# Kernel tuning notes

Measured on AMD Instinct MI355X. Metric: run time of the kernel, lower is better.

## Reference

```python
import jax, jax.numpy as jnp
import numpy as np

B, N, INPUT, HIDDEN, WEIGHT = 1024, 50, 128, 256, 64
NEG_INF = -1.0e9


def setup_inputs() -> dict:
    key = jax.random.key(0)
    ks = jax.random.split(key, 12)
    s_in = 1.0 / np.sqrt(INPUT)
    s_h = 1.0 / np.sqrt(HIDDEN)
    s_w = 1.0 / np.sqrt(WEIGHT)
    return {
        "targets": jax.random.normal(ks[0], (B, N, INPUT), jnp.float32),
        "h0": jax.random.normal(ks[1], (B, HIDDEN), jnp.float32),
        "c0": jax.random.normal(ks[2], (B, HIDDEN), jnp.float32),
        # nn.Linear(input_size, hidden_size)
        "W_enc": jax.random.uniform(ks[3], (HIDDEN, INPUT), jnp.float32, -s_in, s_in),
        "b_enc": jax.random.uniform(ks[4], (HIDDEN,), jnp.float32, -s_in, s_in),
        # nn.LSTMCell(input_size, hidden_size)
        "W_ih": jax.random.uniform(ks[5], (4 * HIDDEN, INPUT), jnp.float32, -s_h, s_h),
        "W_hh": jax.random.uniform(ks[6], (4 * HIDDEN, HIDDEN), jnp.float32, -s_h, s_h),
        "b_ih": jax.random.uniform(ks[7], (4 * HIDDEN,), jnp.float32, -s_h, s_h),
        "b_hh": jax.random.uniform(ks[8], (4 * HIDDEN,), jnp.float32, -s_h, s_h),
        # W1, W2: Linear(hidden, weight, bias=False); vt: Linear(weight, 1, bias=False)
        "W1": jax.random.uniform(ks[9], (WEIGHT, HIDDEN), jnp.float32, -s_h, s_h),
        "W2": jax.random.uniform(ks[10], (WEIGHT, HIDDEN), jnp.float32, -s_h, s_h),
        "vt": jax.random.uniform(ks[11], (WEIGHT,), jnp.float32, -s_w, s_w),
    }


def _lstm_cell(x, h, c, W_ih, W_hh, b_ih, b_hh):
    gates = x @ W_ih.T + h @ W_hh.T + (b_ih + b_hh)  # [B, 4H]
    i, f, g, o = jnp.split(gates, 4, axis=-1)
    i, f, o = jax.nn.sigmoid(i), jax.nn.sigmoid(f), jax.nn.sigmoid(o)
    g = jnp.tanh(g)
    c_new = f * c + i * g
    h_new = o * jnp.tanh(c_new)
    return h_new, c_new


def _pointer_forward(targets, h0, c0, W_enc, b_enc, W_ih, W_hh, b_ih, b_hh, W1, W2, vt):
    b, n, _ = targets.shape
    encoder_states = targets @ W_enc.T + b_enc        # [B, N, H]
    blend1 = encoder_states @ W1.T                    # [B, N, W]
    col = jnp.arange(n)

    def step(carry, _):
        h, c, dec_in, selected = carry
        h, c = _lstm_cell(dec_in, h, c, W_ih, W_hh, b_ih, b_hh)
        blend2 = h @ W2.T                             # [B, W]
        out = jnp.tanh(blend1 + blend2[:, None, :]) @ vt  # [B, N]
        out = jnp.where(selected, NEG_INF, out)
        sel_idx = jnp.argmax(out, axis=-1)            # [B]
        selected = selected | (col[None, :] == sel_idx[:, None])
        p = jnp.maximum(jax.nn.softmax(out, axis=-1), 1e-9)
        dec_in = targets[jnp.arange(b), sel_idx]      # gather next input
        return (h, c, dec_in, selected), p

    dec_in0 = jnp.zeros_like(targets[:, 0])
    selected0 = jnp.zeros((b, n), dtype=bool)
    _, probs = jax.lax.scan(step, (h0, c0, dec_in0, selected0), None, length=n)
    return jnp.transpose(probs, (1, 0, 2))            # [B, N, N]


def reference(targets, h0, c0, W_enc, b_enc, W_ih, W_hh, b_ih, b_hh, W1, W2, vt):
    return _pointer_forward(targets, h0, c0, W_enc, b_enc, W_ih, W_hh, b_ih, b_hh, W1, W2, vt)
```

## Files before the change

kernel.cpp:

```cpp
#include <hip/hip_runtime.h>

#define O_WC     16
#define O_BC     (16 + 8192)
#define O_BIAS   (O_BC + 64)
#define O_BLEND1 16384
#define O_WB     3293184
#define O_XW     4194304
#define XW_FLOATS 52428800ULL
#define NEG_INF_V (-1.0e9f)

#define WB_TILE 12288
#define WB_W2   786432

using bf16x8 = __attribute__((ext_vector_type(8))) __bf16;
using f32x4  = __attribute__((ext_vector_type(4))) float;

__device__ __forceinline__ f32x4 mfma16(bf16x8 a, bf16x8 b, f32x4 c) {
  return __builtin_amdgcn_mfma_f32_16x16x32_bf16(a, b, c, 0, 0, 0);
}

__device__ __forceinline__ float b2f(unsigned int u) {
  union { unsigned int i; float f; } x; x.i = u << 16; return x.f;
}
__device__ __forceinline__ unsigned short f2b(float f) {
  union { float f; unsigned int i; } x; x.f = f;
  unsigned int r = x.i + 0x7fffu + ((x.i >> 16) & 1u);
  return (unsigned short)(r >> 16);
}
__device__ __forceinline__ float ldv(const void* p, int b16, long long i) {
  if (b16) return b2f(((const unsigned short*)p)[i]);
  return ((const float*)p)[i];
}
__device__ __forceinline__ float sigm(float x)  { return 1.0f / (1.0f + __expf(-x)); }
__device__ __forceinline__ float tanhx(float x) { return 1.0f - 2.0f / (1.0f + __expf(2.0f * x)); }

__device__ __forceinline__ float bfsel(const uint4& u, int e) {
  unsigned int w = (e < 2) ? u.x : (e < 4) ? u.y : (e < 6) ? u.z : u.w;
  union { unsigned int i; float f; } x;
  x.i = (e & 1) ? (w & 0xffff0000u) : (w << 16);
  return x.f;
}

__global__ __launch_bounds__(256) void prepAll(
    const void* b_enc, const void* b_ih, const void* b_hh, const void* W1,
    const void* W_ih, const void* W_hh, const void* W2, float* ws) {
  __shared__ int anybig;
  const int t = threadIdx.x;
  const int blk = blockIdx.x;
  if (t == 0) anybig = 0;
  __syncthreads();
  {
    unsigned short u = ((const unsigned short*)b_enc)[t];
    float f = b2f((unsigned int)u);
    if (!(fabsf(f) <= 1.0f)) atomicOr(&anybig, 1);
  }
  __syncthreads();
  const int b16 = anybig ? 0 : 1;

  if (blk == 0) {
    if (t == 0) ((int*)ws)[0] = b16;
    for (int k = t; k < 1024; k += 256)
      ws[O_BIAS + k] = ldv(b_ih, b16, k) + ldv(b_hh, b16, k);
    if (t < 64) {
      float acc = 0.f;
      for (int h = 0; h < 256; ++h)
        acc += ldv(W1, b16, t * 256 + h) * ldv(b_enc, b16, h);
      ws[O_BC + t] = acc;
    }
  }
  if (blk < 32) {
  }
  unsigned short* wb = (unsigned short*)(ws + O_WB);
  const int i = blk * 256 + t;
  {
    int g = i >> 8, k = i & 255;
    int nt = g >> 4, r = g & 15;
    int kc = k >> 5, lane = ((k >> 3) & 3) * 16 + r, e = k & 7;
    float w = ldv(W_hh, b16, i);
    unsigned short hi = f2b(w);
    long long d = (long long)nt * WB_TILE + kc * 512 + lane * 8 + e;
    wb[d] = hi;
    wb[d + 4096] = f2b(w - b2f((unsigned int)hi));
  }
  if (i < 131072) {
    int g = i >> 7, k = i & 127;
    int nt = g >> 4, r = g & 15;
    int kc = k >> 5, lane = ((k >> 3) & 3) * 16 + r, e = k & 7;
    float w = ldv(W_ih, b16, i);
    unsigned short hi = f2b(w);
    long long d = (long long)nt * WB_TILE + 8192 + kc * 512 + lane * 8 + e;
    wb[d] = hi;
    wb[d + 2048] = f2b(w - b2f((unsigned int)hi));
  }
  if (i < 16384) {
    int g = i >> 8, k = i & 255;
    int ntw = g >> 4, r = g & 15;
    int kc = k >> 5, lane = ((k >> 3) & 3) * 16 + r, e = k & 7;
    float w = ldv(W2, b16, i);
    unsigned short hi = f2b(w);
    long long d = WB_W2 + ntw * 8192 + kc * 512 + lane * 8 + e;
    wb[d] = hi;
    wb[d + 4096] = f2b(w - b2f((unsigned int)hi));
  }
}

__global__ void prep1(const void* W_enc, const void* W1, const void* b_enc,
                      float* ws) {
  __shared__ int anybig;
  int t = threadIdx.x;
  if (t == 0) anybig = 0;
  __syncthreads();
  {
    unsigned short u = ((const unsigned short*)b_enc)[t];
    float f = b2f((unsigned int)u);
    if (!(fabsf(f) <= 1.0f)) atomicOr(&anybig, 1);
  }
  __syncthreads();
  int b16 = anybig ? 0 : 1;
  int o = blockIdx.x * 256 + t;
  int w = o >> 7, i = o & 127;
  float acc = 0.f;
  for (int h = 0; h < 256; ++h)
    acc += ldv(W1, b16, w * 256 + h) * ldv(W_enc, b16, h * 128 + i);
  ws[O_WC + o] = acc;
}

__global__ __launch_bounds__(256) void blendk(const void* targets, float* ws) {
  __shared__ float tg[6400];
  __shared__ float wc[8192];
  int b16 = ((const int*)ws)[0];
  int t = threadIdx.x, b = blockIdx.x;
  for (int k = t; k < 8192; k += 256) wc[k] = ws[O_WC + k];
  if (b16) {
    const unsigned short* tp = (const unsigned short*)targets + (long long)b * 6400;
    for (int k = t * 8; k < 6400; k += 2048) {
      uint4 u = *(const uint4*)(tp + k);
      #pragma unroll
      for (int e = 0; e < 8; ++e) tg[k + e] = bfsel(u, e);
    }
  } else {
    const float* tp = (const float*)targets + (long long)b * 6400;
    for (int k = t; k < 6400; k += 256) tg[k] = tp[k];
  }
  __syncthreads();
  int w = t & 63, j0 = t >> 6;
  float bcv = ws[O_BC + w];
  for (int j = j0; j < 50; j += 4) {
    float acc = 0.f;
    for (int i0 = 0; i0 < 128; i0 += 8) {
      const float4* q = (const float4*)(wc + w * 128 + i0);
      float4 a = q[0], bb = q[1];
      const float* x = &tg[j * 128 + i0];
      acc += a.x * x[0] + a.y * x[1] + a.z * x[2] + a.w * x[3]
           + bb.x * x[4] + bb.y * x[5] + bb.z * x[6] + bb.w * x[7];
    }
    ws[O_BLEND1 + (b * 50 + j) * 64 + w] = acc + bcv;
  }
}

__global__ __launch_bounds__(512)
__attribute__((amdgpu_waves_per_eu(2, 2)))
void xwK(const void* targets, float* ws) {
  __shared__ __align__(16) unsigned short tgS[4][32][264];
  const int b16 = ((const int*)ws)[0];
  const int t = threadIdx.x;
  const int b0 = blockIdx.x * 4;
  const unsigned short* wb = (const unsigned short*)(ws + O_WB);
  float* xwp = ws + O_XW;
  const int l = t & 63, Wv = t >> 6, lr = l & 15, hc = l >> 4;

  #pragma unroll 1
  for (int half = 0; half < 2; ++half) {
    __syncthreads();
    for (int k = t; k < 4 * 32 * 128; k += 512) {
      int p = k >> 12, jr = (k >> 7) & 31, i = k & 127;
      int j = half * 32 + jr;
      float v = (j < 50) ? ldv(targets, b16, ((long long)(b0 + p) * 50 + j) * 128 + i)
                         : 0.f;
      unsigned short hi = f2b(v);
      tgS[p][jr][i]       = hi;
      tgS[p][jr][128 + i] = f2b(v - b2f((unsigned int)hi));
    }
    __syncthreads();
    const int njg = (half == 0) ? 4 : 3;
    #pragma unroll 1
    for (int ti = 0; ti < 8; ++ti) {
      const int nt = Wv * 8 + ti;
      const unsigned short* tb = wb + (long long)nt * WB_TILE + 8192 + l * 8;
      bf16x8 wih[8];
      #pragma unroll
      for (int kc = 0; kc < 4; ++kc) {
        wih[kc]     = *(const bf16x8*)(tb + kc * 512);
        wih[4 + kc] = *(const bf16x8*)(tb + 2048 + kc * 512);
      }
      #pragma unroll 1
      for (int p = 0; p < 4; ++p) {
        #pragma unroll 1
        for (int jh = 0; jh < njg; ++jh) {
          bf16x8 ax[4];
          const unsigned short* tp =
              &tgS[p][jh * 8 + (lr & 7)][((lr < 8) ? 0 : 128) + hc * 8];
          #pragma unroll
          for (int kc = 0; kc < 4; ++kc) ax[kc] = *(const bf16x8*)(tp + kc * 32);
          f32x4 cH = {0.f,0.f,0.f,0.f}, cL = {0.f,0.f,0.f,0.f};
          #pragma unroll
          for (int kc = 0; kc < 4; ++kc) {
            cH = mfma16(ax[kc], wih[kc], cH);
            cL = mfma16(ax[kc], wih[4 + kc], cL);
          }
          f32x4 acc = cH + cL;
          float s0 = acc[0] + __shfl_xor(acc[0], 32, 64);
          float s1 = acc[1] + __shfl_xor(acc[1], 32, 64);
          float s2 = acc[2] + __shfl_xor(acc[2], 32, 64);
          float s3 = acc[3] + __shfl_xor(acc[3], 32, 64);
          if (l < 32) {
            int jb = half * 32 + jh * 8 + hc * 4;
            long long ro = (long long)(b0 + p) * 50;
            if (jb + 0 < 50) xwp[(ro + jb + 0) * 1024 + nt * 16 + lr] = s0;
            if (jb + 1 < 50) xwp[(ro + jb + 1) * 1024 + nt * 16 + lr] = s1;
            if (jb + 2 < 50) xwp[(ro + jb + 2) * 1024 + nt * 16 + lr] = s2;
            if (jb + 3 < 50) xwp[(ro + jb + 3) * 1024 + nt * 16 + lr] = s3;
          }
        }
      }
    }
  }
}

__global__ __launch_bounds__(1024)
__attribute__((amdgpu_waves_per_eu(4, 4)))
void mainX(const void* targets, const void* h0, const void* c0, const void* vt,
           float* ws, void* outp) {
  __shared__ __align__(16) unsigned short hS[16][264];
  __shared__ __align__(16) float xwS[4][1024];
  __shared__ float cT[4][256];
  __shared__ float gsh[4][1024];
  __shared__ float bias_s[1024];
  __shared__ float b2s[4][64];
  __shared__ float outs[4][64];
  __shared__ float vt_s[64];
  __shared__ int   selidx[4];
  __shared__ int   selb[4][64];

  const int b16 = ((const int*)ws)[0];
  const int t = threadIdx.x;
  const int bbase = blockIdx.x * 4;
  const unsigned short* wb = (const unsigned short*)(ws + O_WB);
  const float* xw = ws + O_XW;

  bias_s[t & 1023] = ws[O_BIAS + (t & 1023)];
  if (t < 64) vt_s[t] = ldv(vt, b16, t);
  if (t < 256) selb[t >> 6][t & 63] = 0;
  if (t < 4) selidx[t] = -1;
  {
    unsigned short* z1 = &hS[0][0];
    for (int k = t; k < 16 * 264; k += 1024) z1[k] = 0;
  }
  __syncthreads();
  {
    int p = t >> 8, j = t & 255;
    float h = ldv(h0, b16, (long long)(bbase + p) * 256 + j);
    float c = ldv(c0, b16, (long long)(bbase + p) * 256 + j);
    unsigned short hi = f2b(h);
    hS[p][j]     = hi;
    hS[p + 4][j] = f2b(h - b2f((unsigned int)hi));
    cT[p][j]     = c;
  }
  __syncthreads();

  const int l  = t & 63, Wv = t >> 6;
  const int lr = l & 15, hc = l >> 4;

  float bl1[16];
  int cp = 0, cj = 0, cq = 0;
  if (t < 800) {
    int o = t >> 2; cq = t & 3;
    cp = o / 50; cj = o - cp * 50;
    const float* bl = ws + O_BLEND1 + (((long long)(bbase + cp) * 50 + cj) * 64) + cq * 16;
    #pragma unroll
    for (int v4 = 0; v4 < 4; ++v4) {
      float4 bv = *(const float4*)(bl + v4 * 4);
      bl1[v4 * 4 + 0] = bv.x; bl1[v4 * 4 + 1] = bv.y;
      bl1[v4 * 4 + 2] = bv.z; bl1[v4 * 4 + 3] = bv.w;
    }
  } else {
    #pragma unroll
    for (int e = 0; e < 16; ++e) bl1[e] = 0.f;
  }

  #pragma unroll 1
  for (int step = 0; step < 50; ++step) {
    {
      bf16x8 ah[8];
      #pragma unroll
      for (int kc = 0; kc < 8; ++kc)
        ah[kc] = *(const bf16x8*)&hS[lr][kc * 32 + hc * 8];
      #pragma unroll 1
      for (int ti = 0; ti < 4; ++ti) {
        const int nt = Wv * 4 + ti;
        const unsigned short* tb = wb + (long long)nt * WB_TILE + l * 8;
        bf16x8 wh[4], wl[4];
        #pragma unroll
        for (int q2 = 0; q2 < 4; ++q2) {
          wh[q2] = *(const bf16x8*)(tb + q2 * 512);
          wl[q2] = *(const bf16x8*)(tb + 4096 + q2 * 512);
        }
        f32x4 aH = {0.f,0.f,0.f,0.f}, aL = {0.f,0.f,0.f,0.f};
        #pragma unroll
        for (int kc = 0; kc < 8; ++kc) {
          const int cur = kc & 3;
          aH = mfma16(ah[kc], wh[cur], aH);
          aL = mfma16(ah[kc], wl[cur], aL);
          if (kc + 4 < 8) {
            wh[cur] = *(const bf16x8*)(tb + (kc + 4) * 512);
            wl[cur] = *(const bf16x8*)(tb + 4096 + (kc + 4) * 512);
          }
        }
        f32x4 acc = aH + aL;
        float s0 = acc[0] + __shfl_xor(acc[0], 16, 64);
        float s1 = acc[1] + __shfl_xor(acc[1], 16, 64);
        float s2 = acc[2] + __shfl_xor(acc[2], 16, 64);
        float s3 = acc[3] + __shfl_xor(acc[3], 16, 64);
        if (l < 16) {
          const int g = nt * 16 + l;
          gsh[0][g] = s0; gsh[1][g] = s1; gsh[2][g] = s2; gsh[3][g] = s3;
        }
      }
    }
    __syncthreads();

    {
      int j = t & 255, p = t >> 8;
      float gi = gsh[p][j], gf = gsh[p][256 + j];
      float gg = gsh[p][512 + j], go = gsh[p][768 + j];
      if (selidx[p] >= 0) {
        gi += xwS[p][j]; gf += xwS[p][256 + j];
        gg += xwS[p][512 + j]; go += xwS[p][768 + j];
      }
      gi = sigm (gi + bias_s[j]);
      gf = sigm (gf + bias_s[256 + j]);
      gg = tanhx(gg + bias_s[512 + j]);
      go = sigm (go + bias_s[768 + j]);
      float c = gf * cT[p][j] + gi * gg;
      cT[p][j] = c;
      float h = go * tanhx(c);
      unsigned short hi = f2b(h);
      hS[p][j]     = hi;
      hS[p + 4][j] = f2b(h - b2f((unsigned int)hi));
    }
    __syncthreads();

    if (Wv < 4) {
      bf16x8 bh[8];
      #pragma unroll
      for (int kc = 0; kc < 8; ++kc)
        bh[kc] = *(const bf16x8*)&hS[lr][kc * 32 + hc * 8];
      const unsigned short* tb2 = wb + WB_W2 + Wv * 8192 + l * 8;
      f32x4 cH = {0.f,0.f,0.f,0.f}, cL = {0.f,0.f,0.f,0.f};
      #pragma unroll
      for (int kc = 0; kc < 8; ++kc) {
        cH = mfma16(bh[kc], *(const bf16x8*)(tb2 + kc * 512), cH);
        cL = mfma16(bh[kc], *(const bf16x8*)(tb2 + 4096 + kc * 512), cL);
      }
      f32x4 acc = cH + cL;
      float s0 = acc[0] + __shfl_xor(acc[0], 16, 64);
      float s1 = acc[1] + __shfl_xor(acc[1], 16, 64);
      float s2 = acc[2] + __shfl_xor(acc[2], 16, 64);
      float s3 = acc[3] + __shfl_xor(acc[3], 16, 64);
      if (l < 16) {
        const int g = Wv * 16 + l;
        b2s[0][g] = s0; b2s[1][g] = s1; b2s[2][g] = s2; b2s[3][g] = s3;
      }
    }
    __syncthreads();

    if (t < 800) {
      float acc = 0.f;
      #pragma unroll
      for (int e = 0; e < 16; ++e) {
        int w0 = cq * 16 + e;
        acc += vt_s[w0] * tanhx(bl1[e] + b2s[cp][w0]);
      }
      acc += __shfl_xor(acc, 1, 64);
      acc += __shfl_xor(acc, 2, 64);
      if (cq == 0) outs[cp][cj] = selb[cp][cj] ? NEG_INF_V : acc;
    }
    __syncthreads();

    if (Wv < 4) {
      int p = Wv, lane = l;
      float v = (lane < 50) ? outs[p][lane] : -3.4e38f;
      int idx = lane;
      #pragma unroll
      for (int msk = 1; msk < 64; msk <<= 1) {
        float ov = __shfl_xor(v, msk, 64);
        int   oi = __shfl_xor(idx, msk, 64);
        if (ov > v || (ov == v && oi < idx)) { v = ov; idx = oi; }
      }
      {
        const float* xr = xw + ((long long)(bbase + p) * 50 + idx) * 1024;
        #pragma unroll
        for (int kk = 0; kk < 4; ++kk)
          *(float4*)&xwS[p][lane * 4 + kk * 256] =
              *(const float4*)(xr + lane * 4 + kk * 256);
      }
      float e = (lane < 50) ? __expf(outs[p][lane] - v) : 0.f;
      float ssum = e;
      #pragma unroll
      for (int msk = 1; msk < 64; msk <<= 1) ssum += __shfl_xor(ssum, msk, 64);
      if (lane < 50) {
        float prob = fmaxf(e / ssum, 1e-9f);
        long long o = (long long)(bbase + p) * 2500 + step * 50 + lane;
        if (b16) ((unsigned short*)outp)[o] = f2b(prob);
        else     ((float*)outp)[o] = prob;
      }
      if (lane == 0) selidx[p] = idx;
      if (lane == idx) selb[p][idx] = 1;
    }
    __syncthreads();
  }
}

__global__ __launch_bounds__(512)
__attribute__((amdgpu_waves_per_eu(2, 2)))
void mainK6(const void* targets, const void* h0, const void* c0, const void* vt,
            float* ws, void* outp) {
  __shared__ __align__(16) unsigned short hS[16][264];
  __shared__ __align__(16) unsigned short xA[16][136];
  __shared__ float cT[8][256];
  __shared__ float gsh[8][1024];
  __shared__ float bias_s[1024];
  __shared__ float b2s[8][64];
  __shared__ float outs[8][64];
  __shared__ float vt_s[64];
  __shared__ int   selidx[8];
  __shared__ int   selb[8][64];

  const int b16 = ((const int*)ws)[0];
  const int t = threadIdx.x;
  const int bbase = blockIdx.x * 8;
  const unsigned short* wb = (const unsigned short*)(ws + O_WB);

  for (int k = t; k < 1024; k += 512) bias_s[k] = ws[O_BIAS + k];
  if (t < 64) vt_s[t] = ldv(vt, b16, t);
  if (t < 512) selb[t >> 6][t & 63] = 0;
  if (t < 8) selidx[t] = -1;
  {
    unsigned short* z1 = &hS[0][0];
    unsigned short* z2 = &xA[0][0];
    for (int k = t; k < 16 * 264; k += 512) z1[k] = 0;
    for (int k = t; k < 16 * 136; k += 512) z2[k] = 0;
  }
  __syncthreads();
  for (int k = t; k < 2048; k += 512) {
    int p = k >> 8, j = k & 255;
    float h = ldv(h0, b16, (long long)(bbase + p) * 256 + j);
    float c = ldv(c0, b16, (long long)(bbase + p) * 256 + j);
    unsigned short hi = f2b(h);
    hS[p][j]     = hi;
    hS[p + 8][j] = f2b(h - b2f((unsigned int)hi));
    cT[p][j]     = c;
  }
  __syncthreads();

  const int l  = t & 63, Wv = t >> 6;
  const int lr = l & 15;

  #pragma unroll 1
  for (int step = 0; step < 50; ++step) {
    {
      bf16x8 ah[8], ax[4];
      #pragma unroll
      for (int kc = 0; kc < 8; ++kc)
        ah[kc] = *(const bf16x8*)&hS[lr][kc * 32 + (l >> 4) * 8];
      #pragma unroll
      for (int kc = 0; kc < 4; ++kc)
        ax[kc] = *(const bf16x8*)&xA[lr][kc * 32 + (l >> 4) * 8];
      #pragma unroll 1
      for (int ti = 0; ti < 8; ++ti) {
        const int nt = Wv * 8 + ti;
        const unsigned short* tb = wb + (long long)nt * WB_TILE + l * 8;
        bf16x8 wH[12], wL[12];
        #pragma unroll
        for (int kc = 0; kc < 8; ++kc) {
          wH[kc] = *(const bf16x8*)(tb + kc * 512);
          wL[kc] = *(const bf16x8*)(tb + 4096 + kc * 512);
        }
        #pragma unroll
        for (int kc = 0; kc < 4; ++kc) {
          wH[8 + kc] = *(const bf16x8*)(tb + 8192 + kc * 512);
          wL[8 + kc] = *(const bf16x8*)(tb + 10240 + kc * 512);
        }
        f32x4 aH = {0.f,0.f,0.f,0.f}, aL = {0.f,0.f,0.f,0.f};
        #pragma unroll
        for (int kc = 0; kc < 8; ++kc) {
          aH = mfma16(ah[kc], wH[kc], aH);
          aL = mfma16(ah[kc], wL[kc], aL);
        }
        #pragma unroll
        for (int kc = 0; kc < 4; ++kc) {
          aH = mfma16(ax[kc], wH[8 + kc], aH);
          aL = mfma16(ax[kc], wL[8 + kc], aL);
        }
        f32x4 acc = aH + aL;
        float s0 = acc[0] + __shfl_xor(acc[0], 32, 64);
        float s1 = acc[1] + __shfl_xor(acc[1], 32, 64);
        float s2 = acc[2] + __shfl_xor(acc[2], 32, 64);
        float s3 = acc[3] + __shfl_xor(acc[3], 32, 64);
        if (l < 32) {
          const int g = nt * 16 + (l & 15), pb = (l >> 4) * 4;
          gsh[pb + 0][g] = s0; gsh[pb + 1][g] = s1;
          gsh[pb + 2][g] = s2; gsh[pb + 3][g] = s3;
        }
      }
    }
    __syncthreads();

    for (int k = t; k < 2048; k += 512) {
      int j = k & 255, p = k >> 8;
      float gi = sigm (gsh[p][j]       + bias_s[j]);
      float gf = sigm (gsh[p][256 + j] + bias_s[256 + j]);
      float gg = tanhx(gsh[p][512 + j] + bias_s[512 + j]);
      float go = sigm (gsh[p][768 + j] + bias_s[768 + j]);
      float c = gf * cT[p][j] + gi * gg;
      cT[p][j] = c;
      float h = go * tanhx(c);
      unsigned short hi = f2b(h);
      hS[p][j]     = hi;
      hS[p + 8][j] = f2b(h - b2f((unsigned int)hi));
    }
    __syncthreads();

    if (Wv < 4) {
      bf16x8 bh[8];
      #pragma unroll
      for (int kc = 0; kc < 8; ++kc)
        bh[kc] = *(const bf16x8*)&hS[lr][kc * 32 + (l >> 4) * 8];
      const unsigned short* tb = wb + WB_W2 + Wv * 8192 + l * 8;
      f32x4 aH = {0.f,0.f,0.f,0.f}, aL = {0.f,0.f,0.f,0.f};
      #pragma unroll
      for (int kc = 0; kc < 8; ++kc) {
        aH = mfma16(bh[kc], *(const bf16x8*)(tb + kc * 512), aH);
        aL = mfma16(bh[kc], *(const bf16x8*)(tb + 4096 + kc * 512), aL);
      }
      f32x4 acc = aH + aL;
      float s0 = acc[0] + __shfl_xor(acc[0], 32, 64);
      float s1 = acc[1] + __shfl_xor(acc[1], 32, 64);
      float s2 = acc[2] + __shfl_xor(acc[2], 32, 64);
      float s3 = acc[3] + __shfl_xor(acc[3], 32, 64);
      if (l < 32) {
        const int g = Wv * 16 + (l & 15), pb = (l >> 4) * 4;
        b2s[pb + 0][g] = s0; b2s[pb + 1][g] = s1;
        b2s[pb + 2][g] = s2; b2s[pb + 3][g] = s3;
      }
    }
    __syncthreads();

    if (t < 400) {
      int p = t / 50, j = t - p * 50;
      const float* bl = ws + O_BLEND1 + (((bbase + p) * 50 + j) * 64);
      float acc = 0.f;
      #pragma unroll
      for (int v4 = 0; v4 < 16; ++v4) {
        float4 bv = *(const float4*)(bl + v4 * 4);
        int w0 = v4 * 4;
        acc += vt_s[w0 + 0] * tanhx(bv.x + b2s[p][w0 + 0]);
        acc += vt_s[w0 + 1] * tanhx(bv.y + b2s[p][w0 + 1]);
        acc += vt_s[w0 + 2] * tanhx(bv.z + b2s[p][w0 + 2]);
        acc += vt_s[w0 + 3] * tanhx(bv.w + b2s[p][w0 + 3]);
      }
      outs[p][j] = selb[p][j] ? NEG_INF_V : acc;
    }
    __syncthreads();

    {
      int p = Wv, lane = l;
      float v = (lane < 50) ? outs[p][lane] : -3.4e38f;
      int idx = lane;
      #pragma unroll
      for (int msk = 1; msk < 64; msk <<= 1) {
        float ov = __shfl_xor(v, msk, 64);
        int   oi = __shfl_xor(idx, msk, 64);
        if (ov > v || (ov == v && oi < idx)) { v = ov; idx = oi; }
      }
      float e = (lane < 50) ? __expf(outs[p][lane] - v) : 0.f;
      float ssum = e;
      #pragma unroll
      for (int msk = 1; msk < 64; msk <<= 1) ssum += __shfl_xor(ssum, msk, 64);
      if (lane < 50) {
        float prob = fmaxf(e / ssum, 1e-9f);
        int o = (bbase + p) * 2500 + step * 50 + lane;
        if (b16) ((unsigned short*)outp)[o] = f2b(prob);
        else     ((float*)outp)[o] = prob;
      }
      if (lane == 0) selidx[p] = idx;
      if (lane == idx) selb[p][idx] = 1;
    }
    __syncthreads();

    for (int k = t; k < 1024; k += 512) {
      int p = k >> 7, i = k & 127;
      float xf = ldv(targets, b16,
                     ((long long)(bbase + p) * 50 + selidx[p]) * 128 + i);
      unsigned short hi = f2b(xf);
      xA[p][i]     = hi;
      xA[p + 8][i] = f2b(xf - b2f((unsigned int)hi));
    }
    __syncthreads();
  }
}

extern "C" void kernel_launch(void* const* d_in, const int* in_sizes, int n_in,
                              void* d_out, int out_size, void* d_ws, size_t ws_size,
                              hipStream_t stream) {
  (void)in_sizes; (void)n_in; (void)out_size;
  const void* targets = d_in[0];
  const void* h0      = d_in[1];
  const void* c0      = d_in[2];
  const void* W_enc   = d_in[3];
  const void* b_enc   = d_in[4];
  const void* W_ih    = d_in[5];
  const void* W_hh    = d_in[6];
  const void* b_ih    = d_in[7];
  const void* b_hh    = d_in[8];
  const void* W1      = d_in[9];
  const void* W2      = d_in[10];
  const void* vt      = d_in[11];
  float* ws = (float*)d_ws;

  int use_xw = (ws_size >= ((size_t)O_XW + (size_t)XW_FLOATS) * 4) ? 1 : 0;

  prepAll<<<1024, 256, 0, stream>>>(b_enc, b_ih, b_hh, W1, W_ih, W_hh, W2, ws);
  prep1<<<32, 256, 0, stream>>>(W_enc, W1, b_enc, ws);
  blendk<<<1024, 256, 0, stream>>>(targets, ws);
  if (use_xw) {
    xwK<<<256, 512, 0, stream>>>(targets, ws);
    mainX<<<256, 1024, 0, stream>>>(targets, h0, c0, vt, ws, d_out);
  } else {
    mainK6<<<128, 512, 0, stream>>>(targets, h0, c0, vt, ws, d_out);
  }
}
```

Measured before the change: 991.8 us.

## Overlap next-step recurrent GEMM with attention/softmax via warp specialization

Splits the 16 waves of mainX into two groups. 12 waves compute the next step's h·W_hh gate GEMM while 4 waves compute blend2, the attention scores, argmax, softmax and the gather. The small group synchronises internally through a shared-memory atomic counter with spin-sleep, which removes several block-wide barriers per step. Blend1 is staged in shared memory instead of per-thread registers, and the first step's GEMM is hoisted before the loop. The costs are more shared memory use, a spin-wait, and more score work per lane (64 tanh per lane instead of 16).

```diff
diff --git a/kernel.cpp b/kernel.cpp
--- a/kernel.cpp
+++ b/kernel.cpp
@@ -67,8 +67,6 @@
         acc += ldv(W1, b16, t * 256 + h) * ldv(b_enc, b16, h);
       ws[O_BC + t] = acc;
     }
-  }
-  if (blk < 32) {
   }
   unsigned short* wb = (unsigned short*)(ws + O_WB);
   const int i = blk * 256 + t;
@@ -233,14 +231,15 @@
            float* ws, void* outp) {
   __shared__ __align__(16) unsigned short hS[16][264];
   __shared__ __align__(16) float xwS[4][1024];
+  __shared__ float bl1S[4][50][66];
   __shared__ float cT[4][256];
   __shared__ float gsh[4][1024];
   __shared__ float bias_s[1024];
   __shared__ float b2s[4][64];
-  __shared__ float outs[4][64];
   __shared__ float vt_s[64];
   __shared__ int   selidx[4];
   __shared__ int   selb[4][64];
+  __shared__ int   auxcnt;
 
   const int b16 = ((const int*)ws)[0];
   const int t = threadIdx.x;
@@ -248,13 +247,18 @@
   const unsigned short* wb = (const unsigned short*)(ws + O_WB);
   const float* xw = ws + O_XW;
 
-  bias_s[t & 1023] = ws[O_BIAS + (t & 1023)];
+  bias_s[t] = ws[O_BIAS + t];
   if (t < 64) vt_s[t] = ldv(vt, b16, t);
   if (t < 256) selb[t >> 6][t & 63] = 0;
   if (t < 4) selidx[t] = -1;
+  if (t == 0) auxcnt = 0;
   {
     unsigned short* z1 = &hS[0][0];
     for (int k = t; k < 16 * 264; k += 1024) z1[k] = 0;
+  }
+  for (int k = t; k < 12800; k += 1024) {
+    int p = k / 3200, r = k - p * 3200, j = r >> 6, w = r & 63;
+    bl1S[p][j][w] = ws[O_BLEND1 + (((long long)(bbase + p) * 50 + j) << 6) + w];
   }
   __syncthreads();
   {
@@ -271,64 +275,46 @@
   const int l  = t & 63, Wv = t >> 6;
   const int lr = l & 15, hc = l >> 4;
 
-  float bl1[16];
-  int cp = 0, cj = 0, cq = 0;
-  if (t < 800) {
-    int o = t >> 2; cq = t & 3;
-    cp = o / 50; cj = o - cp * 50;
-    const float* bl = ws + O_BLEND1 + (((long long)(bbase + cp) * 50 + cj) * 64) + cq * 16;
+  {
+    bf16x8 ah[8];
     #pragma unroll
-    for (int v4 = 0; v4 < 4; ++v4) {
-      float4 bv = *(const float4*)(bl + v4 * 4);
-      bl1[v4 * 4 + 0] = bv.x; bl1[v4 * 4 + 1] = bv.y;
-      bl1[v4 * 4 + 2] = bv.z; bl1[v4 * 4 + 3] = bv.w;
-    }
-  } else {
-    #pragma unroll
-    for (int e = 0; e < 16; ++e) bl1[e] = 0.f;
-  }
+    for (int kc = 0; kc < 8; ++kc)
+      ah[kc] = *(const bf16x8*)&hS[lr][kc * 32 + hc * 8];
+    #pragma unroll 1
+    for (int nt = Wv; nt < 64; nt += 16) {
+      const unsigned short* tb = wb + (long long)nt * WB_TILE + l * 8;
+      bf16x8 wh[4], wl[4];
+      #pragma unroll
+      for (int q2 = 0; q2 < 4; ++q2) {
+        wh[q2] = *(const bf16x8*)(tb + q2 * 512);
+        wl[q2] = *(const bf16x8*)(tb + 4096 + q2 * 512);
+      }
+      f32x4 aH = {0.f,0.f,0.f,0.f}, aL = {0.f,0.f,0.f,0.f};
+      #pragma unroll
+      for (int kc = 0; kc < 8; ++kc) {
+        const int cur = kc & 3;
+        aH = mfma16(ah[kc], wh[cur], aH);
+        aL = mfma16(ah[kc], wl[cur], aL);
+        if (kc + 4 < 8) {
+          wh[cur] = *(const bf16x8*)(tb + (kc + 4) * 512);
+          wl[cur] = *(const bf16x8*)(tb + 4096 + (kc + 4) * 512);
+        }
+      }
+      f32x4 acc = aH + aL;
+      float s0 = acc[0] + __shfl_xor(acc[0], 16, 64);
+      float s1 = acc[1] + __shfl_xor(acc[1], 16, 64);
+      float s2 = acc[2] + __shfl_xor(acc[2], 16, 64);
+      float s3 = acc[3] + __shfl_xor(acc[3], 16, 64);
+      if (l < 16) {
+        const int g = nt * 16 + l;
+        gsh[0][g] = s0; gsh[1][g] = s1; gsh[2][g] = s2; gsh[3][g] = s3;
+      }
+    }
+  }
+  __syncthreads();
 
   #pragma unroll 1
   for (int step = 0; step < 50; ++step) {
-    {
-      bf16x8 ah[8];
-      #pragma unroll
-      for (int kc = 0; kc < 8; ++kc)
-        ah[kc] = *(const bf16x8*)&hS[lr][kc * 32 + hc * 8];
-      #pragma unroll 1
-      for (int ti = 0; ti < 4; ++ti) {
-        const int nt = Wv * 4 + ti;
-        const unsigned short* tb = wb + (long long)nt * WB_TILE + l * 8;
-        bf16x8 wh[4], wl[4];
-        #pragma unroll
-        for (int q2 = 0; q2 < 4; ++q2) {
-          wh[q2] = *(const bf16x8*)(tb + q2 * 512);
-          wl[q2] = *(const bf16x8*)(tb + 4096 + q2 * 512);
-        }
-        f32x4 aH = {0.f,0.f,0.f,0.f}, aL = {0.f,0.f,0.f,0.f};
-        #pragma unroll
-        for (int kc = 0; kc < 8; ++kc) {
-          const int cur = kc & 3;
-          aH = mfma16(ah[kc], wh[cur], aH);
-          aL = mfma16(ah[kc], wl[cur], aL);
-          if (kc + 4 < 8) {
-            wh[cur] = *(const bf16x8*)(tb + (kc + 4) * 512);
-            wl[cur] = *(const bf16x8*)(tb + 4096 + (kc + 4) * 512);
-          }
-        }
-        f32x4 acc = aH + aL;
-        float s0 = acc[0] + __shfl_xor(acc[0], 16, 64);
-        float s1 = acc[1] + __shfl_xor(acc[1], 16, 64);
-        float s2 = acc[2] + __shfl_xor(acc[2], 16, 64);
-        float s3 = acc[3] + __shfl_xor(acc[3], 16, 64);
-        if (l < 16) {
-          const int g = nt * 16 + l;
-          gsh[0][g] = s0; gsh[1][g] = s1; gsh[2][g] = s2; gsh[3][g] = s3;
-        }
-      }
-    }
-    __syncthreads();
-
     {
       int j = t & 255, p = t >> 8;
       float gi = gsh[p][j], gf = gsh[p][256 + j];
@@ -350,72 +336,112 @@
     }
     __syncthreads();
 
-    if (Wv < 4) {
-      bf16x8 bh[8];
-      #pragma unroll
-      for (int kc = 0; kc < 8; ++kc)
-        bh[kc] = *(const bf16x8*)&hS[lr][kc * 32 + hc * 8];
-      const unsigned short* tb2 = wb + WB_W2 + Wv * 8192 + l * 8;
-      f32x4 cH = {0.f,0.f,0.f,0.f}, cL = {0.f,0.f,0.f,0.f};
-      #pragma unroll
-      for (int kc = 0; kc < 8; ++kc) {
-        cH = mfma16(bh[kc], *(const bf16x8*)(tb2 + kc * 512), cH);
-        cL = mfma16(bh[kc], *(const bf16x8*)(tb2 + 4096 + kc * 512), cL);
-      }
-      f32x4 acc = cH + cL;
-      float s0 = acc[0] + __shfl_xor(acc[0], 16, 64);
-      float s1 = acc[1] + __shfl_xor(acc[1], 16, 64);
-      float s2 = acc[2] + __shfl_xor(acc[2], 16, 64);
-      float s3 = acc[3] + __shfl_xor(acc[3], 16, 64);
-      if (l < 16) {
-        const int g = Wv * 16 + l;
-        b2s[0][g] = s0; b2s[1][g] = s1; b2s[2][g] = s2; b2s[3][g] = s3;
-      }
-    }
-    __syncthreads();
-
-    if (t < 800) {
-      float acc = 0.f;
-      #pragma unroll
-      for (int e = 0; e < 16; ++e) {
-        int w0 = cq * 16 + e;
-        acc += vt_s[w0] * tanhx(bl1[e] + b2s[cp][w0]);
-      }
-      acc += __shfl_xor(acc, 1, 64);
-      acc += __shfl_xor(acc, 2, 64);
-      if (cq == 0) outs[cp][cj] = selb[cp][cj] ? NEG_INF_V : acc;
-    }
-    __syncthreads();
-
-    if (Wv < 4) {
-      int p = Wv, lane = l;
-      float v = (lane < 50) ? outs[p][lane] : -3.4e38f;
-      int idx = lane;
-      #pragma unroll
-      for (int msk = 1; msk < 64; msk <<= 1) {
-        float ov = __shfl_xor(v, msk, 64);
-        int   oi = __shfl_xor(idx, msk, 64);
-        if (ov > v || (ov == v && oi < idx)) { v = ov; idx = oi; }
-      }
+    if (Wv >= 4) {
+      if (step < 49) {
+        bf16x8 ah[8];
+        #pragma unroll
+        for (int kc = 0; kc < 8; ++kc)
+          ah[kc] = *(const bf16x8*)&hS[lr][kc * 32 + hc * 8];
+        #pragma unroll 1
+        for (int nt = Wv - 4; nt < 64; nt += 12) {
+          const unsigned short* tb = wb + (long long)nt * WB_TILE + l * 8;
+          bf16x8 wh[4], wl[4];
+          #pragma unroll
+          for (int q2 = 0; q2 < 4; ++q2) {
+            wh[q2] = *(const bf16x8*)(tb + q2 * 512);
+            wl[q2] = *(const bf16x8*)(tb + 4096 + q2 * 512);
+          }
+          f32x4 aH = {0.f,0.f,0.f,0.f}, aL = {0.f,0.f,0.f,0.f};
+          #pragma unroll
+          for (int kc = 0; kc < 8; ++kc) {
+            const int cur = kc & 3;
+            aH = mfma16(ah[kc], wh[cur], aH);
+            aL = mfma16(ah[kc], wl[cur], aL);
+            if (kc + 4 < 8) {
+              wh[cur] = *(const bf16x8*)(tb + (kc + 4) * 512);
+              wl[cur] = *(const bf16x8*)(tb + 4096 + (kc + 4) * 512);
+            }
+          }
+          f32x4 acc = aH + aL;
+          float s0 = acc[0] + __shfl_xor(acc[0], 16, 64);
+          float s1 = acc[1] + __shfl_xor(acc[1], 16, 64);
+          float s2 = acc[2] + __shfl_xor(acc[2], 16, 64);
+          float s3 = acc[3] + __shfl_xor(acc[3], 16, 64);
+          if (l < 16) {
+            const int g = nt * 16 + l;
+            gsh[0][g] = s0; gsh[1][g] = s1; gsh[2][g] = s2; gsh[3][g] = s3;
+          }
+        }
+      }
+    } else {
       {
-        const float* xr = xw + ((long long)(bbase + p) * 50 + idx) * 1024;
-        #pragma unroll
-        for (int kk = 0; kk < 4; ++kk)
-          *(float4*)&xwS[p][lane * 4 + kk * 256] =
-              *(const float4*)(xr + lane * 4 + kk * 256);
-      }
-      float e = (lane < 50) ? __expf(outs[p][lane] - v) : 0.f;
-      float ssum = e;
-      #pragma unroll
-      for (int msk = 1; msk < 64; msk <<= 1) ssum += __shfl_xor(ssum, msk, 64);
-      if (lane < 50) {
-        float prob = fmaxf(e / ssum, 1e-9f);
-        long long o = (long long)(bbase + p) * 2500 + step * 50 + lane;
-        if (b16) ((unsigned short*)outp)[o] = f2b(prob);
-        else     ((float*)outp)[o] = prob;
-      }
-      if (lane == 0) selidx[p] = idx;
-      if (lane == idx) selb[p][idx] = 1;
+        bf16x8 bh[8];
+        #pragma unroll
+        for (int kc = 0; kc < 8; ++kc)
+          bh[kc] = *(const bf16x8*)&hS[lr][kc * 32 + hc * 8];
+        const unsigned short* tb2 = wb + WB_W2 + Wv * 8192 + l * 8;
+        f32x4 cH = {0.f,0.f,0.f,0.f}, cL = {0.f,0.f,0.f,0.f};
+        #pragma unroll
+        for (int kc = 0; kc < 8; ++kc) {
+          cH = mfma16(bh[kc], *(const bf16x8*)(tb2 + kc * 512), cH);
+          cL = mfma16(bh[kc], *(const bf16x8*)(tb2 + 4096 + kc * 512), cL);
+        }
+        f32x4 acc = cH + cL;
+        float s0 = acc[0] + __shfl_xor(acc[0], 16, 64);
+        float s1 = acc[1] + __shfl_xor(acc[1], 16, 64);
+        float s2 = acc[2] + __shfl_xor(acc[2], 16, 64);
+        float s3 = acc[3] + __shfl_xor(acc[3], 16, 64);
+        if (l < 16) {
+          const int g = Wv * 16 + l;
+          b2s[0][g] = s0; b2s[1][g] = s1; b2s[2][g] = s2; b2s[3][g] = s3;
+        }
+      }
+      __threadfence_block();
+      if (l == 0)
+        __hip_atomic_fetch_add(&auxcnt, 1, __ATOMIC_RELEASE,
+                               __HIP_MEMORY_SCOPE_WORKGROUP);
+      while (__hip_atomic_load(&auxcnt, __ATOMIC_ACQUIRE,
+                               __HIP_MEMORY_SCOPE_WORKGROUP) < 4 * (step + 1))
+        __builtin_amdgcn_s_sleep(2);
+
+      {
+        const int p = Wv, lane = l;
+        float outv = -3.4e38f;
+        if (lane < 50) {
+          float acc = 0.f;
+          #pragma unroll 8
+          for (int w = 0; w < 64; ++w)
+            acc += vt_s[w] * tanhx(bl1S[p][lane][w] + b2s[p][w]);
+          outv = selb[p][lane] ? NEG_INF_V : acc;
+        }
+        float v = outv;
+        int idx = lane;
+        #pragma unroll
+        for (int msk = 1; msk < 64; msk <<= 1) {
+          float ov = __shfl_xor(v, msk, 64);
+          int   oi = __shfl_xor(idx, msk, 64);
+          if (ov > v || (ov == v && oi < idx)) { v = ov; idx = oi; }
+        }
+        {
+          const float* xr = xw + ((long long)(bbase + p) * 50 + idx) * 1024;
+          #pragma unroll
+          for (int kk = 0; kk < 4; ++kk)
+            *(float4*)&xwS[p][lane * 4 + kk * 256] =
+                *(const float4*)(xr + lane * 4 + kk * 256);
+        }
+        float e = (lane < 50) ? __expf(outv - v) : 0.f;
+        float ssum = e;
+        #pragma unroll
+        for (int msk = 1; msk < 64; msk <<= 1) ssum += __shfl_xor(ssum, msk, 64);
+        if (lane < 50) {
+          float prob = fmaxf(e / ssum, 1e-9f);
+          long long o = (long long)(bbase + p) * 2500 + step * 50 + lane;
+          if (b16) ((unsigned short*)outp)[o] = f2b(prob);
+          else     ((float*)outp)[o] = prob;
+        }
+        if (lane == 0) selidx[p] = idx;
+        if (lane == idx) selb[p][idx] = 1;
+      }
     }
     __syncthreads();
   }
```

New measurement: 856.1 us. 1.16x faster.
